# Kernel optimization log

Hardware: AMD Instinct MI355X
Metric: run time of the kernel (lower is better)

The kernel has to match this reference:

```python
import jax, jax.numpy as jnp
import numpy as np

B, N, F_IN, F_OUT = 16, 128, 128, 128
E_OUT, B_IN, B_OUT = 16, 16, 16
CI, L1_OUT = 64, 256
NEG = -9e15


def _lstm_dir(x, Wih, Whh, bih, bhh, reverse=False):
    # x: [B, T, D]; torch gate order i, f, g, o
    Bx, T, _ = x.shape
    H = Whh.shape[1]
    xs = jnp.flip(x, 1) if reverse else x
    pre = xs @ Wih.T + bih + bhh  # [B, T, 4H]

    def step(carry, p):
        h, c = carry
        g = p + h @ Whh.T
        i, f, gg, o = jnp.split(g, 4, axis=-1)
        c = jax.nn.sigmoid(f) * c + jax.nn.sigmoid(i) * jnp.tanh(gg)
        h = jax.nn.sigmoid(o) * jnp.tanh(c)
        return (h, c), h

    h0 = jnp.zeros((Bx, H), x.dtype)
    _, hs = jax.lax.scan(step, (h0, h0), jnp.swapaxes(pre, 0, 1))
    hs = jnp.swapaxes(hs, 0, 1)  # [B, T, H]
    return jnp.flip(hs, 1) if reverse else hs


def setup_inputs() -> dict:
    key = jax.random.key(0)
    ks = jax.random.split(key, 20)
    s = 0.1
    inp = {
        "input": jax.random.normal(ks[0], (B, N, F_IN), jnp.float32),
        "adj": jax.random.randint(ks[1], (B, N, N), 0, 2).astype(jnp.int32),
        "weight": jax.random.normal(ks[2], (B, N, N, B_IN), jnp.float32),
        "W": jax.random.normal(ks[3], (F_IN, F_OUT), jnp.float32) * s,
        "a": jax.random.normal(ks[4], (2 * F_OUT, E_OUT), jnp.float32) * s,
        "W_wf": jax.random.normal(ks[5], (B_OUT, B_IN), jnp.float32) * s,
        "b_wf": jax.random.normal(ks[6], (B_OUT,), jnp.float32) * s,
        "W_fc": jax.random.normal(ks[7], (E_OUT + B_OUT,), jnp.float32) * s,
        "b_fc": jax.random.normal(ks[8], (), jnp.float32) * s,
        "W_fcc": jax.random.normal(ks[9], (F_OUT,), jnp.float32) * s,
        "b_fcc": jax.random.normal(ks[10], (), jnp.float32) * s,
        "W_out": jax.random.normal(ks[11], (L1_OUT, 2 * CI + F_OUT), jnp.float32) * s,
        "b_out": jax.random.normal(ks[12], (L1_OUT,), jnp.float32) * s,
        "Wih_f": jax.random.normal(ks[13], (4 * CI, N), jnp.float32) * s,
        "Whh_f": jax.random.normal(ks[14], (4 * CI, CI), jnp.float32) * s,
        "bih_f": jax.random.normal(ks[15], (4 * CI,), jnp.float32) * s,
        "bhh_f": jax.random.normal(ks[16], (4 * CI,), jnp.float32) * s,
        "Wih_b": jax.random.normal(ks[17], (4 * CI, N), jnp.float32) * s,
        "Whh_b": jax.random.normal(ks[18], (4 * CI, CI), jnp.float32) * s,
        "bih_b": jax.random.normal(ks[19], (4 * CI,), jnp.float32) * s,
        "bhh_b": jax.random.normal(jax.random.fold_in(key, 99), (4 * CI,), jnp.float32) * s,
    }
    return inp


def reference(input, adj, weight, W, a, W_wf, b_wf, W_fc, b_fc, W_fcc, b_fcc,
              W_out, b_out, Wih_f, Whh_f, bih_f, bhh_f, Wih_b, Whh_b, bih_b, bhh_b):
    h = input @ W  # [B, N, F_OUT]
    # faithful replication of torch repeat/cat/view (interleaved pairing)
    A = jnp.tile(h, (1, 1, N)).reshape(B, N * N, F_OUT)
    B2 = jnp.tile(h, (1, N, 1))  # [B, N*N, F]
    atom_trans = jnp.concatenate([A, B2], axis=1).reshape(B, N, N, 2 * F_OUT)
    e = atom_trans @ a  # [B, N, N, E_OUT]
    w = weight @ W_wf.T + b_wf  # [B, N, N, B_OUT]
    e = jax.nn.leaky_relu(jnp.concatenate([e, w], axis=3))
    e = jnp.einsum('bijd,d->bij', e, W_fc) + b_fc  # fc -> squeeze
    attention = jax.nn.softmax(jnp.where(adj > 0, e, NEG), axis=2)
    # dropout p=0 (eval) -> identity
    at_input = attention[..., None] * h[:, :, None, :]  # [B, N, N, F]
    hn = jax.nn.leaky_relu(jnp.einsum('bijf,f->bij', at_input, W_fcc) + b_fcc)
    hf = _lstm_dir(hn, Wih_f, Whh_f, bih_f, bhh_f, reverse=False)
    hb = _lstm_dir(hn, Wih_b, Whh_b, bih_b, bhh_b, reverse=True)
    hn = jax.nn.leaky_relu(jnp.concatenate([hf, hb], axis=-1))  # [B, N, 2*CI]
    h1 = jnp.einsum('bij,bjf->bif', attention, h)  # [B, N, F]
    h1 = jnp.concatenate([hn, h1], axis=2)  # [B, N, 2*CI+F]
    out = jnp.einsum('bnd,od->bno', h1, W_out) + b_out
    return jax.nn.elu(out)
```

## Files before the change

kernel.cpp:

```cpp
#include <hip/hip_runtime.h>
#include <math.h>

#define B 16
#define N 128
#define F 128
#define CI 64
#define NEG (-9e15f)

__device__ __forceinline__ float lrelu(float x){ return x > 0.f ? x : 0.01f*x; }
__device__ __forceinline__ float fastrcp(float x){ return __builtin_amdgcn_rcpf(x); }
__device__ __forceinline__ float sigm(float x){ return fastrcp(1.f + __expf(-x)); }
__device__ __forceinline__ float tanh_f(float x){ return 1.f - 2.f*fastrcp(__expf(2.f*x) + 1.f); }
__device__ __forceinline__ float rdlane(float v, int l) {
    return __int_as_float(__builtin_amdgcn_readlane(__float_as_int(v), l));
}

__global__ __launch_bounds__(128) void k1_h(const float* __restrict__ input,
        const float* __restrict__ W, const float* __restrict__ a,
        const float* __restrict__ W_fcc,
        float* __restrict__ h, float* __restrict__ ha1, float* __restrict__ ha2,
        float* __restrict__ hw) {
    int row = blockIdx.x;
    int t = threadIdx.x;
    __shared__ float x[F];
    __shared__ float hr[F];
    x[t] = input[row*F + t];
    __syncthreads();
    float acc = 0.f;
    #pragma unroll
    for (int k = 0; k < F; k++) acc += x[k] * W[k*F + t];
    h[row*F + t] = acc;
    hr[t] = acc;
    __syncthreads();
    if (t < 16) {
        float a1 = 0.f;
        #pragma unroll
        for (int f = 0; f < F; f++) a1 += hr[f] * a[f*16 + t];
        ha1[row*16 + t] = a1;
    } else if (t < 32) {
        int e = t - 16;
        float a2 = 0.f;
        #pragma unroll
        for (int f = 0; f < F; f++) a2 += hr[f] * a[(F+f)*16 + e];
        ha2[row*16 + e] = a2;
    } else if (t == 32) {
        float s = 0.f;
        #pragma unroll
        for (int f = 0; f < F; f++) s += hr[f] * W_fcc[f];
        hw[row] = s;
    }
}

__global__ __launch_bounds__(128) void k2_att(
        const float* __restrict__ ha1, const float* __restrict__ ha2,
        const float* __restrict__ weight, const int* __restrict__ adj,
        const float* __restrict__ W_wf, const float* __restrict__ b_wf,
        const float* __restrict__ W_fc, const float* __restrict__ b_fc,
        const float* __restrict__ b_fcc, const float* __restrict__ hw,
        const float* __restrict__ h,
        float* __restrict__ hn, float* __restrict__ h1) {
    int b  = blockIdx.x >> 6;
    int ic = blockIdx.x & 63;
    int j = threadIdx.x;
    int lane = j & 63, wid = j >> 6;
    __shared__ float att_lds[2][N];
    __shared__ float red[2];
    float bfc = b_fc[0], bfcc = b_fcc[0];
    #pragma unroll 1
    for (int ii = 0; ii < 2; ii++) {
        int i = ic*2 + ii;
        int r1, r2;
        if (i < 64) { r1 = 2*i + (j >= 64 ? 1 : 0); r2 = r1; }
        else        { r1 = (2*j) & 127; r2 = r1 + 1; }
        const float4* p1 = (const float4*)(ha1 + (b*N + r1)*16);
        const float4* p2 = (const float4*)(ha2 + (b*N + r2)*16);
        float e16[16];
        #pragma unroll
        for (int q = 0; q < 4; q++) {
            float4 v1 = p1[q], v2 = p2[q];
            e16[q*4+0]=v1.x+v2.x; e16[q*4+1]=v1.y+v2.y;
            e16[q*4+2]=v1.z+v2.z; e16[q*4+3]=v1.w+v2.w;
        }
        const float4* wv4 = (const float4*)(weight + ((size_t)((b*N+i)*N) + j)*16);
        float wvec[16];
        #pragma unroll
        for (int q = 0; q < 4; q++) {
            float4 v = wv4[q];
            wvec[q*4]=v.x; wvec[q*4+1]=v.y; wvec[q*4+2]=v.z; wvec[q*4+3]=v.w;
        }
        float val = bfc;
        #pragma unroll
        for (int e = 0; e < 16; e++) val += lrelu(e16[e]) * W_fc[e];
        #pragma unroll
        for (int o = 0; o < 16; o++) {
            float acc = b_wf[o];
            #pragma unroll
            for (int k = 0; k < 16; k++) acc += wvec[k] * W_wf[o*16 + k];
            val += lrelu(acc) * W_fc[16 + o];
        }
        int av = adj[(b*N+i)*N + j];
        float logit = av > 0 ? val : NEG;
        float m = logit;
        #pragma unroll
        for (int off = 32; off > 0; off >>= 1) m = fmaxf(m, __shfl_xor(m, off));
        if (lane == 0) red[wid] = m;
        __syncthreads();
        m = fmaxf(red[0], red[1]);
        __syncthreads();
        float ex = __expf(logit - m);
        float s = ex;
        #pragma unroll
        for (int off = 32; off > 0; off >>= 1) s += __shfl_xor(s, off);
        if (lane == 0) red[wid] = s;
        __syncthreads();
        s = red[0] + red[1];
        __syncthreads();
        float att = ex / s;
        att_lds[ii][j] = att;
        hn[(b*N+i)*N + j] = lrelu(att * hw[b*N+i] + bfcc);
    }
    __syncthreads();
    float acc[2];
    #pragma unroll
    for (int ii = 0; ii < 2; ii++) acc[ii] = 0.f;
    for (int jj = 0; jj < N; jj++) {
        float hv = h[(b*N + jj)*F + j];
        #pragma unroll
        for (int ii = 0; ii < 2; ii++) acc[ii] += att_lds[ii][jj] * hv;
    }
    #pragma unroll
    for (int ii = 0; ii < 2; ii++) h1[(b*N + ic*2 + ii)*F + j] = acc[ii];
}

__global__ __launch_bounds__(256) void k4_pre(
        const float* __restrict__ hn,
        const float* __restrict__ Wih_f, const float* __restrict__ bih_f, const float* __restrict__ bhh_f,
        const float* __restrict__ Wih_b, const float* __restrict__ bih_b, const float* __restrict__ bhh_b,
        float* __restrict__ pre_f, float* __restrict__ pre_b) {
    int dir = blockIdx.y;
    int g = threadIdx.x;
    const float* Wih = dir ? Wih_b : Wih_f;
    float bias = dir ? (bih_b[g] + bhh_b[g]) : (bih_f[g] + bhh_f[g]);
    float* pre = dir ? pre_b : pre_f;
    int r0 = blockIdx.x * 16;
    __shared__ float hl[16][F];
    const float4* src = (const float4*)(hn + (size_t)r0*F);
    float4* dst = (float4*)(&hl[0][0]);
    dst[g] = src[g];
    dst[g+256] = src[g+256];
    __syncthreads();
    float acc[16];
    #pragma unroll
    for (int t = 0; t < 16; t++) acc[t] = bias;
    for (int jc = 0; jc < F; jc += 16) {
        float w[16];
        const float4* wp = (const float4*)(Wih + g*F + jc);
        #pragma unroll
        for (int q = 0; q < 4; q++) {
            float4 v = wp[q];
            w[q*4]=v.x; w[q*4+1]=v.y; w[q*4+2]=v.z; w[q*4+3]=v.w;
        }
        #pragma unroll
        for (int t = 0; t < 16; t++) {
            #pragma unroll
            for (int jj = 0; jj < 16; jj++) acc[t] += hl[t][jc+jj] * w[jj];
        }
    }
    #pragma unroll
    for (int t = 0; t < 16; t++) pre[(size_t)(r0+t)*256 + g] = acc[t];
}

__global__ __launch_bounds__(256) void k5_lstm(
        const float* __restrict__ pre_f, const float* __restrict__ pre_b,
        const float* __restrict__ Whh_f, const float* __restrict__ Whh_b,
        float* __restrict__ hf, float* __restrict__ hb) {
    int b = blockIdx.x;
    int dir = blockIdx.y;
    const float* pre = dir ? pre_b : pre_f;
    const float* Whh = dir ? Whh_b : Whh_f;
    float* hout = dir ? hb : hf;
    int g = threadIdx.x;
    int lane = g & 63;
    float w[CI];
    const float4* wp = (const float4*)(Whh + g*CI);
    #pragma unroll
    for (int q = 0; q < CI/4; q++) {
        float4 v = wp[q];
        w[q*4]=v.x; w[q*4+1]=v.y; w[q*4+2]=v.z; w[q*4+3]=v.w;
    }
    __shared__ float gate[2][256];
    float hreg = 0.f;
    float c = 0.f;
    int tt = dir ? (N-1) : 0;
    int step = dir ? -1 : 1;
    float pnext = pre[((size_t)b*N + tt)*256 + g];
    int buf = 0;
    for (int t = 0; t < N; t++) {
        float a0 = pnext, a1 = 0.f, a2 = 0.f, a3 = 0.f;
        if (t < N-1) pnext = pre[((size_t)b*N + tt + step)*256 + g];
        #pragma unroll
        for (int k = 0; k < CI; k += 4) {
            a0 += rdlane(hreg, k+0) * w[k+0];
            a1 += rdlane(hreg, k+1) * w[k+1];
            a2 += rdlane(hreg, k+2) * w[k+2];
            a3 += rdlane(hreg, k+3) * w[k+3];
        }
        gate[buf][g] = (a0 + a1) + (a2 + a3);
        __syncthreads();
        float ig = gate[buf][lane];
        float fg = gate[buf][CI + lane];
        float gg = gate[buf][2*CI + lane];
        float og = gate[buf][3*CI + lane];
        c = sigm(fg)*c + sigm(ig)*tanh_f(gg);
        float hv = sigm(og)*tanh_f(c);
        hreg = hv;
        if (g < CI) hout[((size_t)b*N + tt)*CI + lane] = hv;
        buf ^= 1;
        tt += step;
    }
}

__global__ __launch_bounds__(256) void k6_out(
        const float* __restrict__ hf, const float* __restrict__ hb,
        const float* __restrict__ h1, const float* __restrict__ W_out,
        const float* __restrict__ b_out, float* __restrict__ out) {
    int r0 = blockIdx.x * 8;
    int o = threadIdx.x;
    __shared__ float rl[8][256];
    #pragma unroll
    for (int rr = 0; rr < 8; rr++) {
        int row = r0 + rr;
        float v;
        if (o < 64)       v = lrelu(hf[row*CI + o]);
        else if (o < 128) v = lrelu(hb[row*CI + (o-64)]);
        else              v = h1[row*F + (o-128)];
        rl[rr][o] = v;
    }
    __syncthreads();
    float acc[8];
    float bo = b_out[o];
    #pragma unroll
    for (int rr = 0; rr < 8; rr++) acc[rr] = bo;
    for (int dc = 0; dc < 256; dc += 16) {
        float w[16];
        const float4* wp = (const float4*)(W_out + o*256 + dc);
        #pragma unroll
        for (int q = 0; q < 4; q++) {
            float4 v = wp[q];
            w[q*4]=v.x; w[q*4+1]=v.y; w[q*4+2]=v.z; w[q*4+3]=v.w;
        }
        #pragma unroll
        for (int rr = 0; rr < 8; rr++) {
            #pragma unroll
            for (int jj = 0; jj < 16; jj++) acc[rr] += rl[rr][dc+jj] * w[jj];
        }
    }
    #pragma unroll
    for (int rr = 0; rr < 8; rr++) {
        float x = acc[rr];
        out[(size_t)(r0+rr)*256 + o] = x > 0.f ? x : (__expf(x) - 1.f);
    }
}

extern "C" void kernel_launch(void* const* d_in, const int* in_sizes, int n_in,
                              void* d_out, int out_size, void* d_ws, size_t ws_size,
                              hipStream_t stream) {
    const float* input = (const float*)d_in[0];
    const int*   adj   = (const int*)  d_in[1];
    const float* weight= (const float*)d_in[2];
    const float* W     = (const float*)d_in[3];
    const float* a     = (const float*)d_in[4];
    const float* W_wf  = (const float*)d_in[5];
    const float* b_wf  = (const float*)d_in[6];
    const float* W_fc  = (const float*)d_in[7];
    const float* b_fc  = (const float*)d_in[8];
    const float* W_fcc = (const float*)d_in[9];
    const float* b_fcc = (const float*)d_in[10];
    const float* W_out = (const float*)d_in[11];
    const float* b_out = (const float*)d_in[12];
    const float* Wih_f = (const float*)d_in[13];
    const float* Whh_f = (const float*)d_in[14];
    const float* bih_f = (const float*)d_in[15];
    const float* bhh_f = (const float*)d_in[16];
    const float* Wih_b = (const float*)d_in[17];
    const float* Whh_b = (const float*)d_in[18];
    const float* bih_b = (const float*)d_in[19];
    const float* bhh_b = (const float*)d_in[20];

    float* ws = (float*)d_ws;
    float* h    = ws;
    float* ha1  = ws + 262144;
    float* ha2  = ws + 294912;
    float* hw   = ws + 327680;
    float* hn   = ws + 329728;
    float* h1   = ws + 591872;
    float* pre_f= ws + 854016;
    float* pre_b= ws + 1378304;
    float* hf   = ws + 1902592;
    float* hb   = ws + 2033664;

    k1_h<<<B*N, 128, 0, stream>>>(input, W, a, W_fcc, h, ha1, ha2, hw);
    k2_att<<<B*64, 128, 0, stream>>>(ha1, ha2, weight, adj, W_wf, b_wf, W_fc,
                                     b_fc, b_fcc, hw, h, hn, h1);
    k4_pre<<<dim3(128, 2), 256, 0, stream>>>(hn, Wih_f, bih_f, bhh_f,
                                             Wih_b, bih_b, bhh_b, pre_f, pre_b);
    k5_lstm<<<dim3(B, 2), 256, 0, stream>>>(pre_f, pre_b, Whh_f, Whh_b, hf, hb);
    k6_out<<<256, 256, 0, stream>>>(hf, hb, h1, W_out, b_out, (float*)d_out);
}
```

Before: 229.7 us.

## Run LSTM recurrence in a single wavefront with per-lane four-gate accumulation

```diff
diff --git a/kernel.cpp b/kernel.cpp
--- a/kernel.cpp
+++ b/kernel.cpp
@@ -143,6 +143,7 @@
     float bias = dir ? (bih_b[g] + bhh_b[g]) : (bih_f[g] + bhh_f[g]);
     float* pre = dir ? pre_b : pre_f;
     int r0 = blockIdx.x * 16;
+    int oidx = (g & 63)*4 + (g >> 6);
     __shared__ float hl[16][F];
     const float4* src = (const float4*)(hn + (size_t)r0*F);
     float4* dst = (float4*)(&hl[0][0]);
@@ -167,10 +168,10 @@
         }
     }
     #pragma unroll
-    for (int t = 0; t < 16; t++) pre[(size_t)(r0+t)*256 + g] = acc[t];
-}
-
-__global__ __launch_bounds__(256) void k5_lstm(
+    for (int t = 0; t < 16; t++) pre[(size_t)(r0+t)*256 + oidx] = acc[t];
+}
+
+__global__ __launch_bounds__(64, 1) void k5_lstm(
         const float* __restrict__ pre_f, const float* __restrict__ pre_b,
         const float* __restrict__ Whh_f, const float* __restrict__ Whh_b,
         float* __restrict__ hf, float* __restrict__ hb) {
@@ -179,43 +180,46 @@
     const float* pre = dir ? pre_b : pre_f;
     const float* Whh = dir ? Whh_b : Whh_f;
     float* hout = dir ? hb : hf;
-    int g = threadIdx.x;
-    int lane = g & 63;
-    float w[CI];
-    const float4* wp = (const float4*)(Whh + g*CI);
-    #pragma unroll
-    for (int q = 0; q < CI/4; q++) {
-        float4 v = wp[q];
-        w[q*4]=v.x; w[q*4+1]=v.y; w[q*4+2]=v.z; w[q*4+3]=v.w;
-    }
-    __shared__ float gate[2][256];
+    int e = threadIdx.x;
+    float2 wif[CI], wgo[CI];
+    {
+        const float4* pi = (const float4*)(Whh + (size_t)(0*CI + e)*CI);
+        const float4* pf = (const float4*)(Whh + (size_t)(1*CI + e)*CI);
+        const float4* pg = (const float4*)(Whh + (size_t)(2*CI + e)*CI);
+        const float4* po = (const float4*)(Whh + (size_t)(3*CI + e)*CI);
+        #pragma unroll
+        for (int q = 0; q < CI/4; q++) {
+            float4 vi = pi[q], vf = pf[q], vg = pg[q], vo = po[q];
+            wif[q*4+0] = make_float2(vi.x, vf.x); wgo[q*4+0] = make_float2(vg.x, vo.x);
+            wif[q*4+1] = make_float2(vi.y, vf.y); wgo[q*4+1] = make_float2(vg.y, vo.y);
+            wif[q*4+2] = make_float2(vi.z, vf.z); wgo[q*4+2] = make_float2(vg.z, vo.z);
+            wif[q*4+3] = make_float2(vi.w, vf.w); wgo[q*4+3] = make_float2(vg.w, vo.w);
+        }
+    }
     float hreg = 0.f;
     float c = 0.f;
     int tt = dir ? (N-1) : 0;
     int step = dir ? -1 : 1;
-    float pnext = pre[((size_t)b*N + tt)*256 + g];
-    int buf = 0;
+    const float4* prep = (const float4*)pre;
+    float4 pcur = prep[((size_t)b*N + tt)*64 + e];
     for (int t = 0; t < N; t++) {
-        float a0 = pnext, a1 = 0.f, a2 = 0.f, a3 = 0.f;
-        if (t < N-1) pnext = pre[((size_t)b*N + tt + step)*256 + g];
-        #pragma unroll
-        for (int k = 0; k < CI; k += 4) {
-            a0 += rdlane(hreg, k+0) * w[k+0];
-            a1 += rdlane(hreg, k+1) * w[k+1];
-            a2 += rdlane(hreg, k+2) * w[k+2];
-            a3 += rdlane(hreg, k+3) * w[k+3];
-        }
-        gate[buf][g] = (a0 + a1) + (a2 + a3);
-        __syncthreads();
-        float ig = gate[buf][lane];
-        float fg = gate[buf][CI + lane];
-        float gg = gate[buf][2*CI + lane];
-        float og = gate[buf][3*CI + lane];
-        c = sigm(fg)*c + sigm(ig)*tanh_f(gg);
-        float hv = sigm(og)*tanh_f(c);
+        float4 pnext;
+        if (t < N-1) pnext = prep[((size_t)b*N + tt + step)*64 + e];
+        float aif_x = pcur.x, aif_y = pcur.y;
+        float ago_x = pcur.z, ago_y = pcur.w;
+        #pragma unroll
+        for (int k = 0; k < CI; k++) {
+            float sk = rdlane(hreg, k);
+            aif_x += sk * wif[k].x;
+            aif_y += sk * wif[k].y;
+            ago_x += sk * wgo[k].x;
+            ago_y += sk * wgo[k].y;
+        }
+        c = sigm(aif_y)*c + sigm(aif_x)*tanh_f(ago_x);
+        float hv = sigm(ago_y)*tanh_f(c);
         hreg = hv;
-        if (g < CI) hout[((size_t)b*N + tt)*CI + lane] = hv;
-        buf ^= 1;
+        hout[((size_t)b*N + tt)*CI + e] = hv;
+        pcur = pnext;
         tt += step;
     }
 }
@@ -304,6 +308,6 @@
                                      b_fc, b_fcc, hw, h, hn, h1);
     k4_pre<<<dim3(128, 2), 256, 0, stream>>>(hn, Wih_f, bih_f, bhh_f,
                                              Wih_b, bih_b, bhh_b, pre_f, pre_b);
-    k5_lstm<<<dim3(B, 2), 256, 0, stream>>>(pre_f, pre_b, Whh_f, Whh_b, hf, hb);
+    k5_lstm<<<dim3(B, 2), 64, 0, stream>>>(pre_f, pre_b, Whh_f, Whh_b, hf, hb);
     k6_out<<<256, 256, 0, stream>>>(hf, hb, h1, W_out, b_out, (float*)d_out);
 }
```

New measurement: 285.0 us. 1.24x slower.
